# Kernel tuning notes

Measured on AMD Instinct MI355X. Metric: run time of the kernel, lower is better.

The kernel has to match this reference:

```python
import jax, jax.numpy as jnp
import numpy as np

B, N, D = 4, 2048, 1024
H, HD = 16, 64
MAX_SEQ = 4096
INNER = H * HD


def setup_inputs() -> dict:
    key = jax.random.key(0)
    ks = jax.random.split(key, 5)
    s = 0.02
    return {
        "x": jax.random.normal(ks[0], (B, N, D), dtype=jnp.float32),
        "ln_gamma": jnp.ones((D,), jnp.float32),
        "ln_beta": jnp.zeros((D,), jnp.float32),
        "w_qkv": jax.random.normal(ks[1], (D, 3 * INNER), dtype=jnp.float32) * s,
        "w_out": jax.random.normal(ks[2], (INNER, D), dtype=jnp.float32) * s,
        "b_out": jnp.zeros((D,), jnp.float32),
    }


def _rope_tables(n, head_dim):
    inv_freq = 1.0 / (10000.0 ** (jnp.arange(0, head_dim, 2, dtype=jnp.float32) / head_dim))
    pos = jnp.arange(n, dtype=jnp.float32)
    ang = pos[:, None] * inv_freq[None, :]  # [n, hd/2]
    return jnp.sin(ang), jnp.cos(ang)


def reference(x, ln_gamma, ln_beta, w_qkv, w_out, b_out):
    b, n, d = x.shape
    # LayerNorm
    mu = jnp.mean(x, axis=-1, keepdims=True)
    var = jnp.var(x, axis=-1, keepdims=True)
    xn = (x - mu) / jnp.sqrt(var + 1e-5) * ln_gamma + ln_beta
    # QKV projection (no bias)
    qkv = xn @ w_qkv  # [b, n, 3*inner]
    q, k, v = jnp.split(qkv, 3, axis=-1)
    def to_heads(t):
        return t.reshape(b, n, H, HD).transpose(0, 2, 1, 3)  # b h n d
    q, k, v = to_heads(q), to_heads(k), to_heads(v)
    # RoPE (half-split rotation, as in source)
    sin, cos = _rope_tables(n, HD)  # [n, hd/2]
    sin = sin[None, None]
    cos = cos[None, None]
    half = HD // 2
    def rotate(t):
        t1, t2 = t[..., :half], t[..., half:]
        return jnp.concatenate([t1 * cos - t2 * sin, t2 * cos + t1 * sin], axis=-1)
    qr, kr = rotate(q), rotate(k)
    scale = HD ** -0.5
    scores = jnp.einsum('bhid,bhjd->bhij', qr, kr) * scale
    probs = jax.nn.softmax(scores, axis=-1)
    out = jnp.einsum('bhij,bhjd->bhid', probs, v)
    out = out.transpose(0, 2, 1, 3).reshape(b, n, INNER)
    return out @ w_out + b_out
```

## Files before the change

kernel.cpp:

```cpp
#include <hip/hip_runtime.h>
#include <hip/hip_bf16.h>

#define Bb   4
#define Nn   2048
#define Dd   1024
#define Hh   16
#define HDd  64
#define IN3  3072
#define RR   8192


typedef __attribute__((ext_vector_type(8))) short short8;
typedef __attribute__((ext_vector_type(4))) float floatx4;

#define MFMA16(a, b, c) __builtin_amdgcn_mfma_f32_16x16x32_bf16((a), (b), (c), 0, 0, 0)

static __device__ __forceinline__ unsigned short f2bf(float f) {
    union { float f; unsigned int u; } v; v.f = f;
    unsigned int r = v.u + 0x7fffu + ((v.u >> 16) & 1u);
    return (unsigned short)(r >> 16);
}
static __device__ __forceinline__ float bf2f(unsigned short h) {
    union { unsigned int u; float f; } v; v.u = ((unsigned int)h) << 16;
    return v.f;
}

static __device__ __forceinline__ float fast_exp2(float x) {
#if __has_builtin(__builtin_amdgcn_exp2f)
    return __builtin_amdgcn_exp2f(x);
#else
    return exp2f(x);
#endif
}

static __device__ __forceinline__ void sincos_rev(float ang, float& s, float& c) {
#if __has_builtin(__builtin_amdgcn_sinf) && __has_builtin(__builtin_amdgcn_cosf)
    float rev = ang * 0.15915494309189535f;
    rev = rev - floorf(rev);
    s = __builtin_amdgcn_sinf(rev);
    c = __builtin_amdgcn_cosf(rev);
#else
    s = sinf(ang);
    c = cosf(ang);
#endif
}

typedef const __attribute__((address_space(1))) void* gas1_t;
typedef __attribute__((address_space(3))) void* las3_t;
static __device__ __forceinline__ void load_lds16(const void* g, void* l) {
    __builtin_amdgcn_global_load_lds((gas1_t)(unsigned long long)g,
                                     (las3_t)(unsigned int)(unsigned long long)l,
                                     16, 0, 0);
}

__global__ void transpose_w(const float* __restrict__ src, unsigned short* __restrict__ dst,
                            int rows, int cols) {
    __shared__ float tile[32][33];
    int c0 = blockIdx.x * 32, r0 = blockIdx.y * 32;
    int tx = threadIdx.x, ty = threadIdx.y;
#pragma unroll
    for (int i = 0; i < 4; ++i) tile[ty + 8 * i][tx] = src[(r0 + ty + 8 * i) * cols + c0 + tx];
    __syncthreads();
#pragma unroll
    for (int i = 0; i < 4; ++i) dst[(c0 + ty + 8 * i) * rows + r0 + tx] = f2bf(tile[tx][ty + 8 * i]);
}

__global__ __launch_bounds__(256) void ln_kernel(const float* __restrict__ x,
                                                 const float* __restrict__ g,
                                                 const float* __restrict__ be,
                                                 unsigned short* __restrict__ xn) {
    int row = blockIdx.x, t = threadIdx.x;
    float4 v = ((const float4*)(x + row * Dd))[t];
    float s  = v.x + v.y + v.z + v.w;
    float sq = v.x * v.x + v.y * v.y + v.z * v.z + v.w * v.w;
#pragma unroll
    for (int off = 1; off < 64; off <<= 1) { s += __shfl_xor(s, off); sq += __shfl_xor(sq, off); }
    __shared__ float ps[4], pq2[4];
    int wv = t >> 6;
    if ((t & 63) == 0) { ps[wv] = s; pq2[wv] = sq; }
    __syncthreads();
    s  = ps[0] + ps[1] + ps[2] + ps[3];
    sq = pq2[0] + pq2[1] + pq2[2] + pq2[3];
    float mu   = s * (1.0f / Dd);
    float var  = sq * (1.0f / Dd) - mu * mu;
    float rstd = rsqrtf(var + 1e-5f);
    float4 gg = ((const float4*)g)[t];
    float4 bb = ((const float4*)be)[t];
    ushort4 o;
    o.x = f2bf((v.x - mu) * rstd * gg.x + bb.x);
    o.y = f2bf((v.y - mu) * rstd * gg.y + bb.y);
    o.z = f2bf((v.z - mu) * rstd * gg.z + bb.z);
    o.w = f2bf((v.w - mu) * rstd * gg.w + bb.w);
    ((ushort4*)(xn + row * Dd))[t] = o;
}

__global__ __launch_bounds__(512, 1) void gemm_qkv(const unsigned short* __restrict__ A,
                                                   const unsigned short* __restrict__ Bt,
                                                   unsigned short* __restrict__ qo,
                                                   unsigned short* __restrict__ ko,
                                                   unsigned short* __restrict__ vo) {
    __shared__ unsigned short LDS[49152];
    int r0 = blockIdx.x * 128, c0 = blockIdx.y * 256;
    int tid = threadIdx.x;
    int wv = tid >> 6, lane = tid & 63, l15 = lane & 15, quad = lane >> 4;
    int wm = wv >> 2, wn = wv & 3;

    floatx4 acc[4][4] = {};
    int swz0 = (quad ^ (l15 & 7)) << 3;
    int swz1 = ((4 | quad) ^ (l15 & 7)) << 3;

    auto stageA = [&](int tt) {
        unsigned short* base = &LDS[(tt & 1) * 8192];
        int k0 = tt * 64;
#pragma unroll
        for (int i = 0; i < 2; ++i) {
            int qq = (wv * 2 + i) * 64 + lane;
            int row = qq >> 3, cp = qq & 7;
            int sc = cp ^ (row & 7);
            load_lds16(&A[(r0 + row) * 1024 + k0 + sc * 8], &base[qq * 8]);
        }
    };
    auto stageB = [&](int tt) {
        unsigned short* base = &LDS[16384 + (tt & 1) * 16384];
        int k0 = tt * 64;
#pragma unroll
        for (int i = 0; i < 4; ++i) {
            int qq = (wv * 4 + i) * 64 + lane;
            int row = qq >> 3, cp = qq & 7;
            int sc = cp ^ (row & 7);
            load_lds16(&Bt[(c0 + row) * 1024 + k0 + sc * 8], &base[qq * 8]);
        }
    };

    stageA(0); stageB(0); stageA(1);
    asm volatile("s_waitcnt vmcnt(2)" ::: "memory");
    __builtin_amdgcn_s_barrier();

    for (int t = 0; t < 16; ++t) {
        int abuf = (t & 1) * 8192;
        int bbuf = 16384 + (t & 1) * 16384;
        short8 af[4][2], bf[2][2];

        if (t < 15) stageB(t + 1);
#pragma unroll
        for (int mi = 0; mi < 4; ++mi) {
            af[mi][0] = *(const short8*)&LDS[abuf + (wm * 64 + mi * 16 + l15) * 64 + swz0];
            af[mi][1] = *(const short8*)&LDS[abuf + (wm * 64 + mi * 16 + l15) * 64 + swz1];
        }
#pragma unroll
        for (int ni = 0; ni < 2; ++ni) {
            bf[ni][0] = *(const short8*)&LDS[bbuf + (wn * 64 + ni * 16 + l15) * 64 + swz0];
            bf[ni][1] = *(const short8*)&LDS[bbuf + (wn * 64 + ni * 16 + l15) * 64 + swz1];
        }
        __builtin_amdgcn_s_barrier();
        asm volatile("s_waitcnt lgkmcnt(0)" ::: "memory");
        __builtin_amdgcn_s_setprio(1);
#pragma unroll
        for (int ks = 0; ks < 2; ++ks)
#pragma unroll
            for (int mi = 0; mi < 4; ++mi)
#pragma unroll
                for (int ni = 0; ni < 2; ++ni)
                    acc[mi][ni] = MFMA16(af[mi][ks], bf[ni][ks], acc[mi][ni]);
        __builtin_amdgcn_s_setprio(0);
        __builtin_amdgcn_s_barrier();

        if (t < 14) stageA(t + 2);
#pragma unroll
        for (int ni = 0; ni < 2; ++ni) {
            bf[ni][0] = *(const short8*)&LDS[bbuf + (wn * 64 + 32 + ni * 16 + l15) * 64 + swz0];
            bf[ni][1] = *(const short8*)&LDS[bbuf + (wn * 64 + 32 + ni * 16 + l15) * 64 + swz1];
        }
        __builtin_amdgcn_s_barrier();
        asm volatile("s_waitcnt lgkmcnt(0)" ::: "memory");
        __builtin_amdgcn_s_setprio(1);
#pragma unroll
        for (int ks = 0; ks < 2; ++ks)
#pragma unroll
            for (int mi = 0; mi < 4; ++mi)
#pragma unroll
                for (int ni = 0; ni < 2; ++ni)
                    acc[mi][2 + ni] = MFMA16(af[mi][ks], bf[ni][ks], acc[mi][2 + ni]);
        __builtin_amdgcn_s_setprio(0);
        if (t < 14)       asm volatile("s_waitcnt vmcnt(2)" ::: "memory");
        else if (t == 14) asm volatile("s_waitcnt vmcnt(0)" ::: "memory");
        __builtin_amdgcn_s_barrier();
    }

    if (c0 < 2048) {
        const float crope = 13.287712379549449f / 32.0f;
        float invf0 = fast_exp2(-(float)l15 * crope);
        float invf1 = fast_exp2(-(float)(l15 + 16) * crope);
#pragma unroll
        for (int mi = 0; mi < 4; ++mi)
#pragma unroll
            for (int r2 = 0; r2 < 4; ++r2) {
                int rr = r0 + wm * 64 + mi * 16 + quad * 4 + r2;
                float n = (float)(rr & 2047);
                float s0, c0r, s1, c1r;
                sincos_rev(n * invf0, s0, c0r);
                sincos_rev(n * invf1, s1, c1r);
                float t1a = acc[mi][0][r2], t2a = acc[mi][2][r2];
                acc[mi][0][r2] = t1a * c0r - t2a * s0;
                acc[mi][2][r2] = t2a * c0r + t1a * s0;
                float t1b = acc[mi][1][r2], t2b = acc[mi][3][r2];
                acc[mi][1][r2] = t1b * c1r - t2b * s1;
                acc[mi][3][r2] = t2b * c1r + t1b * s1;
            }
    }
    if (c0 < 1024) {
        const float qsc = 0.125f * 1.4426950408889634f;
#pragma unroll
        for (int mi = 0; mi < 4; ++mi)
#pragma unroll
            for (int ni = 0; ni < 4; ++ni)
#pragma unroll
                for (int r2 = 0; r2 < 4; ++r2) acc[mi][ni][r2] *= qsc;
    }
    unsigned short* outp = (c0 < 1024) ? qo : (c0 < 2048) ? ko : vo;
#pragma unroll
    for (int ni = 0; ni < 4; ++ni) {
        int c = c0 + wn * 64 + ni * 16 + l15;
        int cin = c & 1023;
        int h = cin >> 6, j = cin & 63;
#pragma unroll
        for (int mi = 0; mi < 4; ++mi) {
#pragma unroll
            for (int r2 = 0; r2 < 4; ++r2) {
                int rr = r0 + wm * 64 + mi * 16 + quad * 4 + r2;
                int b = rr >> 11, n = rr & 2047;
                int bh = b * 16 + h;
                outp[(bh * 2048 + n) * 64 + j] = f2bf(acc[mi][ni][r2]);
            }
        }
    }
}

__global__ __launch_bounds__(256) void vtrans(const unsigned short* __restrict__ v,
                                              unsigned short* __restrict__ vt) {
    __shared__ unsigned short T[64][72];
    int bh = blockIdx.y, n0 = blockIdx.x * 64;
    int t = threadIdx.x;
    int nl = t >> 2, c = (t & 3) * 16;
    const unsigned short* src = v + ((bh * 2048) + n0 + nl) * 64 + c;
    *(short8*)&T[nl][c]     = *(const short8*)src;
    *(short8*)&T[nl][c + 8] = *(const short8*)(src + 8);
    __syncthreads();
    int hd = t >> 2, nc = (t & 3) * 16;
    unsigned short tmp[16];
#pragma unroll
    for (int i = 0; i < 16; ++i) {
        int pos = nc + i;
        int blk = pos >> 5, p = pos & 31;
        int kq = (p >> 3) & 3, hh = (p >> 2) & 1, r = p & 3;
        tmp[i] = T[blk * 32 + hh * 16 + kq * 4 + r][hd];
    }
    unsigned short* dst = vt + ((bh * 64) + hd) * 2048 + n0 + nc;
    *(short8*)dst       = *(const short8*)&tmp[0];
    *(short8*)(dst + 8) = *(const short8*)&tmp[8];
}

__global__ __launch_bounds__(256, 2) void attn_kernel(const unsigned short* __restrict__ q,
                                                      const unsigned short* __restrict__ k,
                                                      const unsigned short* __restrict__ vt,
                                                      unsigned short* __restrict__ attn) {
    __shared__ unsigned short KVs[2][2][64 * 64];
    int fid = blockIdx.x;
    int xcd = fid & 7, rest = fid >> 3;
    int qi = rest & 15, bhg = rest >> 4;
    int bh = bhg * 8 + xcd;
    int q0 = qi * 128;
    int tid = threadIdx.x;
    int wave = tid >> 6, lane = tid & 63, l15 = lane & 15, quad = lane >> 4;
    const unsigned short* qb  = q  + bh * (Nn * HDd);
    const unsigned short* kbp = k  + bh * (Nn * HDd);
    const unsigned short* vb  = vt + bh * (HDd * Nn);
    int qbase = q0 + wave * 32;

    short8 bq[2][2];
#pragma unroll
    for (int g = 0; g < 2; ++g) {
        bq[g][0] = *(const short8*)&qb[(qbase + g * 16 + l15) * 64 + quad * 8];
        bq[g][1] = *(const short8*)&qb[(qbase + g * 16 + l15) * 64 + 32 + quad * 8];
    }

    auto stage = [&](int buf, int kb0) {
#pragma unroll
        for (int i = 0; i < 2; ++i) {
            int c = wave * 2 + i;
            int p = c * 64 + lane;
            int row = p >> 3, pr = p & 7;
            int sc = pr ^ (row & 7);
            load_lds16(&kbp[(kb0 + row) * 64 + sc * 8], &KVs[buf][0][p * 8]);
            load_lds16(&vb[row * Nn + kb0 + sc * 8],    &KVs[buf][1][p * 8]);
        }
    };

    floatx4 ot[2][4] = {};
    floatx4 osum[2] = {};
    const floatx4 fz = {0.0f, 0.0f, 0.0f, 0.0f};
    const short8 vones = {(short)0x3F80, (short)0x3F80, (short)0x3F80, (short)0x3F80,
                          (short)0x3F80, (short)0x3F80, (short)0x3F80, (short)0x3F80};
    int swz0 = (quad ^ (l15 & 7)) << 3;
    int swz1 = ((4 | quad) ^ (l15 & 7)) << 3;

    auto body = [&](int cur, int kt) {
        if (kt < 31) stage(cur ^ 1, (kt + 1) * 64);
        const unsigned short* Kc = KVs[cur][0];
        const unsigned short* Vc = KVs[cur][1];
        short8 ka0[4], ka1[4];
#pragma unroll
        for (int mb = 0; mb < 4; ++mb) {
            ka0[mb] = *(const short8*)&Kc[(mb * 16 + l15) * 64 + swz0];
            ka1[mb] = *(const short8*)&Kc[(mb * 16 + l15) * 64 + swz1];
        }
        short8 bv0[4], bv1[4];
#pragma unroll
        for (int ht = 0; ht < 4; ++ht) {
            int row = (ht * 16 + l15) * 64;
            bv0[ht] = *(const short8*)&Vc[row + swz0];
            bv1[ht] = *(const short8*)&Vc[row + swz1];
        }
#pragma unroll
        for (int g = 0; g < 2; ++g) {
            floatx4 st[4];
            __builtin_amdgcn_s_setprio(1);
#pragma unroll
            for (int mb = 0; mb < 4; ++mb) {
                floatx4 z = MFMA16(ka0[mb], bq[g][0], fz);
                st[mb] = MFMA16(ka1[mb], bq[g][1], z);
            }
            __builtin_amdgcn_s_setprio(0);
            short8 pa[2];
#pragma unroll
            for (int c = 0; c < 2; ++c) {
                union { ushort4 u[2]; short8 s; } w;
#pragma unroll
                for (int t2 = 0; t2 < 2; ++t2) {
                    int mb = 2 * c + t2;
                    float p0 = fast_exp2(st[mb][0]);
                    float p1 = fast_exp2(st[mb][1]);
                    float p2 = fast_exp2(st[mb][2]);
                    float p3 = fast_exp2(st[mb][3]);
                    *(__hip_bfloat162*)&w.u[t2].x = __float22bfloat162_rn(float2{p0, p1});
                    *(__hip_bfloat162*)&w.u[t2].z = __float22bfloat162_rn(float2{p2, p3});
                }
                pa[c] = w.s;
            }
            __builtin_amdgcn_s_setprio(1);
            osum[g] = MFMA16(pa[0], vones, osum[g]);
            osum[g] = MFMA16(pa[1], vones, osum[g]);
#pragma unroll
            for (int ht = 0; ht < 4; ++ht) {
                ot[g][ht] = MFMA16(pa[0], bv0[ht], ot[g][ht]);
                ot[g][ht] = MFMA16(pa[1], bv1[ht], ot[g][ht]);
            }
            __builtin_amdgcn_s_setprio(0);
        }
        if (kt < 31) asm volatile("s_waitcnt vmcnt(0)" ::: "memory");
        __builtin_amdgcn_s_barrier();
    };

    stage(0, 0);
    asm volatile("s_waitcnt vmcnt(0)" ::: "memory");
    __builtin_amdgcn_s_barrier();
    for (int kt = 0; kt < 32; kt += 2) {
        body(0, kt);
        body(1, kt + 1);
    }

    int b = bh >> 4, h = bh & 15;
    unsigned short* ob = ((unsigned short*)KVs) + wave * 1152;
#pragma unroll
    for (int g = 0; g < 2; ++g) {
        float il[4];
#pragma unroll
        for (int r = 0; r < 4; ++r) il[r] = 1.0f / osum[g][r];
#pragma unroll
        for (int ht = 0; ht < 4; ++ht)
#pragma unroll
            for (int r = 0; r < 4; ++r)
                ob[(quad * 4 + r) * 72 + ht * 16 + l15] = f2bf(ot[g][ht][r] * il[r]);
        int q_loc = lane >> 2, seg = lane & 3;
        unsigned short* dst = attn + ((long)(b * Nn + q0 + wave * 32 + g * 16 + q_loc)) * 1024 + h * 64 + seg * 16;
        *(short8*)dst       = *(const short8*)&ob[q_loc * 72 + seg * 16];
        *(short8*)(dst + 8) = *(const short8*)&ob[q_loc * 72 + seg * 16 + 8];
    }
}

__global__ __launch_bounds__(512, 1) void gemm_out(const unsigned short* __restrict__ A,
                                                   const unsigned short* __restrict__ Bt,
                                                   const float* __restrict__ bout,
                                                   float* __restrict__ out) {
    __shared__ unsigned short LDS[49152];
    int r0 = blockIdx.x * 128, c0 = blockIdx.y * 256;
    int tid = threadIdx.x;
    int wv = tid >> 6, lane = tid & 63, l15 = lane & 15, quad = lane >> 4;
    int wm = wv >> 2, wn = wv & 3;

    floatx4 acc[4][4] = {};
    int swz0 = (quad ^ (l15 & 7)) << 3;
    int swz1 = ((4 | quad) ^ (l15 & 7)) << 3;

    auto stageA = [&](int tt) {
        unsigned short* base = &LDS[(tt & 1) * 8192];
        int k0 = tt * 64;
#pragma unroll
        for (int i = 0; i < 2; ++i) {
            int qq = (wv * 2 + i) * 64 + lane;
            int row = qq >> 3, cp = qq & 7;
            int sc = cp ^ (row & 7);
            load_lds16(&A[(r0 + row) * 1024 + k0 + sc * 8], &base[qq * 8]);
        }
    };
    auto stageB = [&](int tt) {
        unsigned short* base = &LDS[16384 + (tt & 1) * 16384];
        int k0 = tt * 64;
#pragma unroll
        for (int i = 0; i < 4; ++i) {
            int qq = (wv * 4 + i) * 64 + lane;
            int row = qq >> 3, cp = qq & 7;
            int sc = cp ^ (row & 7);
            load_lds16(&Bt[(c0 + row) * 1024 + k0 + sc * 8], &base[qq * 8]);
        }
    };

    stageA(0); stageB(0); stageA(1);
    asm volatile("s_waitcnt vmcnt(2)" ::: "memory");
    __builtin_amdgcn_s_barrier();

    for (int t = 0; t < 16; ++t) {
        int abuf = (t & 1) * 8192;
        int bbuf = 16384 + (t & 1) * 16384;
        short8 af[4][2], bf[2][2];

        if (t < 15) stageB(t + 1);
#pragma unroll
        for (int mi = 0; mi < 4; ++mi) {
            af[mi][0] = *(const short8*)&LDS[abuf + (wm * 64 + mi * 16 + l15) * 64 + swz0];
            af[mi][1] = *(const short8*)&LDS[abuf + (wm * 64 + mi * 16 + l15) * 64 + swz1];
        }
#pragma unroll
        for (int ni = 0; ni < 2; ++ni) {
            bf[ni][0] = *(const short8*)&LDS[bbuf + (wn * 64 + ni * 16 + l15) * 64 + swz0];
            bf[ni][1] = *(const short8*)&LDS[bbuf + (wn * 64 + ni * 16 + l15) * 64 + swz1];
        }
        __builtin_amdgcn_s_barrier();
        asm volatile("s_waitcnt lgkmcnt(0)" ::: "memory");
        __builtin_amdgcn_s_setprio(1);
#pragma unroll
        for (int ks = 0; ks < 2; ++ks)
#pragma unroll
            for (int mi = 0; mi < 4; ++mi)
#pragma unroll
                for (int ni = 0; ni < 2; ++ni)
                    acc[mi][ni] = MFMA16(af[mi][ks], bf[ni][ks], acc[mi][ni]);
        __builtin_amdgcn_s_setprio(0);
        __builtin_amdgcn_s_barrier();

        if (t < 14) stageA(t + 2);
#pragma unroll
        for (int ni = 0; ni < 2; ++ni) {
            bf[ni][0] = *(const short8*)&LDS[bbuf + (wn * 64 + 32 + ni * 16 + l15) * 64 + swz0];
            bf[ni][1] = *(const short8*)&LDS[bbuf + (wn * 64 + 32 + ni * 16 + l15) * 64 + swz1];
        }
        __builtin_amdgcn_s_barrier();
        asm volatile("s_waitcnt lgkmcnt(0)" ::: "memory");
        __builtin_amdgcn_s_setprio(1);
#pragma unroll
        for (int ks = 0; ks < 2; ++ks)
#pragma unroll
            for (int mi = 0; mi < 4; ++mi)
#pragma unroll
                for (int ni = 0; ni < 2; ++ni)
                    acc[mi][2 + ni] = MFMA16(af[mi][ks], bf[ni][ks], acc[mi][2 + ni]);
        __builtin_amdgcn_s_setprio(0);
        if (t < 14)       asm volatile("s_waitcnt vmcnt(2)" ::: "memory");
        else if (t == 14) asm volatile("s_waitcnt vmcnt(0)" ::: "memory");
        __builtin_amdgcn_s_barrier();
    }

#pragma unroll
    for (int ni = 0; ni < 4; ++ni) {
        int c = c0 + wn * 64 + ni * 16 + l15;
        float bias = bout[c];
#pragma unroll
        for (int mi = 0; mi < 4; ++mi)
#pragma unroll
            for (int r2 = 0; r2 < 4; ++r2) {
                int rr = r0 + wm * 64 + mi * 16 + quad * 4 + r2;
                out[rr * 1024 + c] = acc[mi][ni][r2] + bias;
            }
    }
}

extern "C" void kernel_launch(void* const* d_in, const int* in_sizes, int n_in,
                              void* d_out, int out_size, void* d_ws, size_t ws_size,
                              hipStream_t stream) {
    const float* x    = (const float*)d_in[0];
    const float* g    = (const float*)d_in[1];
    const float* be   = (const float*)d_in[2];
    const float* wqkv = (const float*)d_in[3];
    const float* wout = (const float*)d_in[4];
    const float* bout = (const float*)d_in[5];
    float* out = (float*)d_out;

    char* ws = (char*)d_ws;
    unsigned short* xn    = (unsigned short*)(ws);
    unsigned short* wqkvT = (unsigned short*)(ws + 16777216);
    unsigned short* woutT = (unsigned short*)(ws + 23068672);
    unsigned short* qb    = (unsigned short*)(ws + 25165824);
    unsigned short* kb    = (unsigned short*)(ws + 41943040);
    unsigned short* vt    = (unsigned short*)(ws + 58720256);
    unsigned short* attn  = (unsigned short*)(ws + 75497472);
    unsigned short* vtmp  = attn;

    transpose_w<<<dim3(IN3 / 32, Dd / 32), dim3(32, 8), 0, stream>>>(wqkv, wqkvT, Dd, IN3);
    transpose_w<<<dim3(Dd / 32, Dd / 32), dim3(32, 8), 0, stream>>>(wout, woutT, Dd, Dd);
    ln_kernel<<<RR, 256, 0, stream>>>(x, g, be, xn);
    gemm_qkv<<<dim3(RR / 128, IN3 / 256), 512, 0, stream>>>(xn, wqkvT, qb, kb, vtmp);
    vtrans<<<dim3(Nn / 64, Bb * Hh), 256, 0, stream>>>(vtmp, vt);
    attn_kernel<<<dim3(Nn / 128 * Bb * Hh), 256, 0, stream>>>(qb, kb, vt, attn);
    gemm_out<<<dim3(RR / 128, Dd / 256), 512, 0, stream>>>(attn, woutT, bout, out);
}
```

Before: 260.3 us.

## Fuse V transpose into QKV GEMM, merge weight transposes, triple-buffer attention

The QKV GEMM epilogue now writes V tiles straight into the transposed, permuted layout through LDS, which removes the separate vtrans kernel and its round trip through memory. The two weight-transpose launches are merged into one launch using blockIdx.z. The attention kernel moves from double to triple buffering of K/V tiles with a two-ahead prefetch and a partial vmcnt wait, and launch_bounds occupancy is raised to 3. The larger LDS footprint and occupancy hint may increase register pressure or cause spills.

```diff
diff --git a/kernel.cpp b/kernel.cpp
--- a/kernel.cpp
+++ b/kernel.cpp
@@ -53,8 +53,11 @@
                                      16, 0, 0);
 }
 
-__global__ void transpose_w(const float* __restrict__ src, unsigned short* __restrict__ dst,
-                            int rows, int cols) {
+__global__ void transpose_w(const float* __restrict__ s0, unsigned short* __restrict__ d0,
+                            const float* __restrict__ s1, unsigned short* __restrict__ d1) {
+    const float* src; unsigned short* dst; int cols;
+    if (blockIdx.z == 0) { src = s0; dst = d0; cols = 3072; }
+    else { if (blockIdx.x >= 32) return; src = s1; dst = d1; cols = 1024; }
     __shared__ float tile[32][33];
     int c0 = blockIdx.x * 32, r0 = blockIdx.y * 32;
     int tx = threadIdx.x, ty = threadIdx.y;
@@ -62,7 +65,7 @@
     for (int i = 0; i < 4; ++i) tile[ty + 8 * i][tx] = src[(r0 + ty + 8 * i) * cols + c0 + tx];
     __syncthreads();
 #pragma unroll
-    for (int i = 0; i < 4; ++i) dst[(c0 + ty + 8 * i) * rows + r0 + tx] = f2bf(tile[tx][ty + 8 * i]);
+    for (int i = 0; i < 4; ++i) dst[(c0 + ty + 8 * i) * 1024 + r0 + tx] = f2bf(tile[tx][ty + 8 * i]);
 }
 
 __global__ __launch_bounds__(256) void ln_kernel(const float* __restrict__ x,
@@ -187,7 +190,42 @@
         __builtin_amdgcn_s_barrier();
     }
 
-    if (c0 < 2048) {
+    if (c0 >= 2048) {
+        unsigned short* T2 = LDS;
+#pragma unroll
+        for (int mi = 0; mi < 4; ++mi)
+#pragma unroll
+            for (int ni = 0; ni < 4; ++ni) {
+                ushort4 w4;
+                w4.x = f2bf(acc[mi][ni][0]);
+                w4.y = f2bf(acc[mi][ni][1]);
+                w4.z = f2bf(acc[mi][ni][2]);
+                w4.w = f2bf(acc[mi][ni][3]);
+                int col = wn * 64 + ni * 16 + l15;
+                int row = wm * 64 + mi * 16 + quad * 4;
+                *(ushort4*)&T2[col * 136 + row] = w4;
+            }
+        __syncthreads();
+        int col = tid >> 1, seg = tid & 1;
+        int hglob = ((c0 - 2048) >> 6) + (col >> 6);
+        int j = col & 63;
+        int b = r0 >> 11;
+        int n0g = (r0 & 2047) + seg * 64;
+        unsigned short tmp[64];
+#pragma unroll
+        for (int gi = 0; gi < 16; ++gi) {
+            int blk = seg * 2 + (gi >> 3);
+            int srow = blk * 32 + 16 * (gi & 1) + 4 * ((gi >> 1) & 3);
+            *(ushort4*)&tmp[gi * 4] = *(const ushort4*)&T2[col * 136 + srow];
+        }
+        unsigned short* dst = vo + (((long)(b * 16 + hglob)) * 64 + j) * 2048 + n0g;
+#pragma unroll
+        for (int k2 = 0; k2 < 8; ++k2)
+            *(short8*)(dst + k2 * 8) = *(const short8*)&tmp[k2 * 8];
+        return;
+    }
+
+    {
         const float crope = 13.287712379549449f / 32.0f;
         float invf0 = fast_exp2(-(float)l15 * crope);
         float invf1 = fast_exp2(-(float)(l15 + 16) * crope);
@@ -217,7 +255,7 @@
 #pragma unroll
                 for (int r2 = 0; r2 < 4; ++r2) acc[mi][ni][r2] *= qsc;
     }
-    unsigned short* outp = (c0 < 1024) ? qo : (c0 < 2048) ? ko : vo;
+    unsigned short* outp = (c0 < 1024) ? qo : ko;
 #pragma unroll
     for (int ni = 0; ni < 4; ++ni) {
         int c = c0 + wn * 64 + ni * 16 + l15;
@@ -236,35 +274,11 @@
     }
 }
 
-__global__ __launch_bounds__(256) void vtrans(const unsigned short* __restrict__ v,
-                                              unsigned short* __restrict__ vt) {
-    __shared__ unsigned short T[64][72];
-    int bh = blockIdx.y, n0 = blockIdx.x * 64;
-    int t = threadIdx.x;
-    int nl = t >> 2, c = (t & 3) * 16;
-    const unsigned short* src = v + ((bh * 2048) + n0 + nl) * 64 + c;
-    *(short8*)&T[nl][c]     = *(const short8*)src;
-    *(short8*)&T[nl][c + 8] = *(const short8*)(src + 8);
-    __syncthreads();
-    int hd = t >> 2, nc = (t & 3) * 16;
-    unsigned short tmp[16];
-#pragma unroll
-    for (int i = 0; i < 16; ++i) {
-        int pos = nc + i;
-        int blk = pos >> 5, p = pos & 31;
-        int kq = (p >> 3) & 3, hh = (p >> 2) & 1, r = p & 3;
-        tmp[i] = T[blk * 32 + hh * 16 + kq * 4 + r][hd];
-    }
-    unsigned short* dst = vt + ((bh * 64) + hd) * 2048 + n0 + nc;
-    *(short8*)dst       = *(const short8*)&tmp[0];
-    *(short8*)(dst + 8) = *(const short8*)&tmp[8];
-}
-
-__global__ __launch_bounds__(256, 2) void attn_kernel(const unsigned short* __restrict__ q,
+__global__ __launch_bounds__(256, 3) void attn_kernel(const unsigned short* __restrict__ q,
                                                       const unsigned short* __restrict__ k,
                                                       const unsigned short* __restrict__ vt,
                                                       unsigned short* __restrict__ attn) {
-    __shared__ unsigned short KVs[2][2][64 * 64];
+    __shared__ unsigned short KVs[3][2][64 * 64];
     int fid = blockIdx.x;
     int xcd = fid & 7, rest = fid >> 3;
     int qi = rest & 15, bhg = rest >> 4;
@@ -304,8 +318,8 @@
     int swz0 = (quad ^ (l15 & 7)) << 3;
     int swz1 = ((4 | quad) ^ (l15 & 7)) << 3;
 
-    auto body = [&](int cur, int kt) {
-        if (kt < 31) stage(cur ^ 1, (kt + 1) * 64);
+    auto body = [&](int cur, int nxt, int kt) {
+        if (kt + 2 < 32) stage(nxt, (kt + 2) * 64);
         const unsigned short* Kc = KVs[cur][0];
         const unsigned short* Vc = KVs[cur][1];
         short8 ka0[4], ka1[4];
@@ -357,17 +371,22 @@
             }
             __builtin_amdgcn_s_setprio(0);
         }
-        if (kt < 31) asm volatile("s_waitcnt vmcnt(0)" ::: "memory");
+        if (kt < 30)       asm volatile("s_waitcnt vmcnt(4)" ::: "memory");
+        else if (kt == 30) asm volatile("s_waitcnt vmcnt(0)" ::: "memory");
         __builtin_amdgcn_s_barrier();
     };
 
     stage(0, 0);
-    asm volatile("s_waitcnt vmcnt(0)" ::: "memory");
+    stage(1, 64);
+    asm volatile("s_waitcnt vmcnt(4)" ::: "memory");
     __builtin_amdgcn_s_barrier();
-    for (int kt = 0; kt < 32; kt += 2) {
-        body(0, kt);
-        body(1, kt + 1);
-    }
+    for (int kt = 0; kt < 30; kt += 3) {
+        body(0, 2, kt);
+        body(1, 0, kt + 1);
+        body(2, 1, kt + 2);
+    }
+    body(0, 2, 30);
+    body(1, 0, 31);
 
     int b = bh >> 4, h = bh & 15;
     unsigned short* ob = ((unsigned short*)KVs) + wave * 1152;
@@ -513,13 +532,10 @@
     unsigned short* kb    = (unsigned short*)(ws + 41943040);
     unsigned short* vt    = (unsigned short*)(ws + 58720256);
     unsigned short* attn  = (unsigned short*)(ws + 75497472);
-    unsigned short* vtmp  = attn;
-
-    transpose_w<<<dim3(IN3 / 32, Dd / 32), dim3(32, 8), 0, stream>>>(wqkv, wqkvT, Dd, IN3);
-    transpose_w<<<dim3(Dd / 32, Dd / 32), dim3(32, 8), 0, stream>>>(wout, woutT, Dd, Dd);
+
+    transpose_w<<<dim3(IN3 / 32, Dd / 32, 2), dim3(32, 8), 0, stream>>>(wqkv, wqkvT, wout, woutT);
     ln_kernel<<<RR, 256, 0, stream>>>(x, g, be, xn);
-    gemm_qkv<<<dim3(RR / 128, IN3 / 256), 512, 0, stream>>>(xn, wqkvT, qb, kb, vtmp);
-    vtrans<<<dim3(Nn / 64, Bb * Hh), 256, 0, stream>>>(vtmp, vt);
+    gemm_qkv<<<dim3(RR / 128, IN3 / 256), 512, 0, stream>>>(xn, wqkvT, qb, kb, vt);
     attn_kernel<<<dim3(Nn / 128 * Bb * Hh), 256, 0, stream>>>(qb, kb, vt, attn);
     gemm_out<<<dim3(RR / 128, Dd / 256), 512, 0, stream>>>(attn, woutT, bout, out);
 }
```

New measurement: 254.3 us. -2.3%, faster.
